# Performance work log

Measured on AMD Instinct MI355X. Metric: run time of the kernel, lower is better.

The kernel has to match this reference:

```python
import jax, jax.numpy as jnp
import numpy as np

DIM = 512
NUM_HEADS = 8


def setup_inputs() -> dict:
    key = jax.random.key(0)
    ks = jax.random.split(key, 10)
    B, N, C = 2, 4096, DIM
    s = 0.02
    return {
        "x": jax.random.normal(ks[0], (B, N, C), dtype=jnp.float32),
        "Wq": jax.random.normal(ks[1], (C, C), dtype=jnp.float32) * s,
        "Wk": jax.random.normal(ks[2], (C, C), dtype=jnp.float32) * s,
        "Wv": jax.random.normal(ks[3], (C, C), dtype=jnp.float32) * s,
        "Wattn": jax.random.normal(ks[4], (C, C), dtype=jnp.float32) * s,
        "Wconv": jax.random.normal(ks[5], (C, C), dtype=jnp.float32) * s,
        "dw_kernel": jax.random.normal(ks[6], (C, 1, 3), dtype=jnp.float32) * s,  # depthwise (O, I/groups, K)
        "dw_bias": jax.random.normal(ks[7], (C,), dtype=jnp.float32) * s,
        "Wcout": jax.random.normal(ks[8], (C, C), dtype=jnp.float32) * s,
        "H": 8,
        "W": 512,
    }


def reference(x, Wq, Wk, Wv, Wattn, Wconv, dw_kernel, dw_bias, Wcout, H, W):
    B, N, C = x.shape
    nh = NUM_HEADS
    hd = C // nh
    scale = hd ** (-0.5)

    # QKV projections (torch Linear: x @ W.T), split heads -> [B, nh, N, hd]
    q = (x @ Wq.T).reshape(B, N, nh, hd).transpose(0, 2, 1, 3)
    k = (x @ Wk.T).reshape(B, N, nh, hd).transpose(0, 2, 1, 3)
    v = (x @ Wv.T).reshape(B, N, nh, hd).transpose(0, 2, 1, 3)

    # Materialized N x N attention (faithful to source)
    scores = jnp.einsum("bhqd,bhkd->bhqk", q, k) * scale
    weights = jax.nn.softmax(scores, axis=-1)
    attn = jnp.einsum("bhqk,bhkd->bhqd", weights, v)
    attn = attn.transpose(0, 2, 1, 3).reshape(B, N, C)
    attn_out = attn @ Wattn.T

    # Parallel depthwise-conv branch
    ci = (x @ Wconv.T).transpose(0, 2, 1)  # [B, C, N]
    co = jax.lax.conv_general_dilated(
        ci, dw_kernel,
        window_strides=(1,), padding=((1, 1),),
        feature_group_count=C,
        dimension_numbers=("NCH", "OIH", "NCH"),
    ) + dw_bias[None, :, None]
    conv_out = co.transpose(0, 2, 1) @ Wcout.T  # [B, N, C]

    out = attn_out + conv_out
    # NOTE: source shadows arg H with num_heads before the view
    return out.reshape(B, nh, W, C)
```

## Files before the change

### kernel.cpp

```cpp
#include <hip/hip_runtime.h>

typedef __attribute__((ext_vector_type(8))) short bf16x8;
typedef __attribute__((ext_vector_type(4))) float f32x4;

constexpr int kB = 2, kN = 4096, kC = 512, kNH = 8, kHD = 64;
constexpr int kBN = kB * kN;
constexpr int kWElems = 262144;
constexpr int kWAll = 6 * kWElems;
constexpr int kWExtra = 3584;
constexpr float kQScale = 0.1803368801f;

__device__ __forceinline__ short f2bf(float f) {
  union { float f; unsigned u; } v; v.f = f;
  unsigned r = v.u + 0x7fffu + ((v.u >> 16) & 1u);
  return (short)(r >> 16);
}
__device__ __forceinline__ float bf2f(short s) {
  union { unsigned u; float f; } v; v.u = ((unsigned)(unsigned short)s) << 16;
  return v.f;
}
__device__ __forceinline__ float exp2_(float x) {
#if __has_builtin(__builtin_amdgcn_exp2f)
  return __builtin_amdgcn_exp2f(x);
#else
  return exp2f(x);
#endif
}
__device__ __forceinline__ unsigned pk2bf(float a, float b) {
  union { float f; unsigned u; } ua, ub; ua.f = a; ub.f = b;
#if __has_builtin(__builtin_amdgcn_perm)
  return __builtin_amdgcn_perm(ub.u + 0x8000u, ua.u + 0x8000u, 0x07060302u);
#else
  return ((ua.u + 0x8000u) >> 16) | (((ub.u + 0x8000u) >> 16) << 16);
#endif
}

__device__ __forceinline__ bf16x8 ld8(const short* p) { return *(const bf16x8*)p; }
__device__ __forceinline__ bf16x8 ld8(const float* p) {
  float4 a = *(const float4*)p;
  float4 b = *(const float4*)(p + 4);
  bf16x8 r;
  r[0] = f2bf(a.x); r[1] = f2bf(a.y); r[2] = f2bf(a.z); r[3] = f2bf(a.w);
  r[4] = f2bf(b.x); r[5] = f2bf(b.y); r[6] = f2bf(b.z); r[7] = f2bf(b.w);
  return r;
}

__device__ __forceinline__ void gload_lds16(const void* g, void* l) {
  __builtin_amdgcn_global_load_lds(
      (const __attribute__((address_space(1))) void*)g,
      (__attribute__((address_space(3))) void*)l, 16, 0, 0);
}

__global__ void detect_dtype(const unsigned* __restrict__ x, int* __restrict__ flag) {
  const int lane = threadIdx.x & 63;
  unsigned w = x[lane];
  int e = (int)((w >> 7) & 0xffu);
  bool bf = (e >= 100 && e <= 140);
  unsigned long long m = __ballot(bf);
  if (lane == 0) *flag = (__popcll(m) >= 32) ? 1 : 0;
}

constexpr int kW8 = kWAll / 8;
constexpr int kX8 = kBN * kC / 8;
__global__ __launch_bounds__(256) void convert_all(
    const void* Wq, const void* Wk, const void* Wv, const void* Wc,
    const void* Wa, const void* Wco, const void* dwk, const void* dwb,
    const void* x, const int* __restrict__ flag, short* __restrict__ dst,
    short* __restrict__ xb) {
  const int gtid = blockIdx.x * 256 + threadIdx.x;
  const bool bf = (*flag != 0);
  if (gtid < kW8) {
    const int e = gtid * 8;
    const int t = e >> 18, off = e & (kWElems - 1);
    const void* src = (t == 0) ? Wq : (t == 1) ? Wk : (t == 2) ? Wv
                    : (t == 3) ? Wc : (t == 4) ? Wa : Wco;
    bf16x8 v = bf ? ld8((const short*)src + off) : ld8((const float*)src + off);
    *(bf16x8*)(dst + e) = v;
  } else if (gtid < kW8 + kWExtra) {
    const int eoff = gtid - kW8;
    if (eoff < 1536) {
      dst[kWAll + eoff] = bf ? ((const short*)dwk)[eoff]
                             : f2bf(((const float*)dwk)[eoff]);
    } else if (eoff < 2048) {
      const int i = eoff - 1536;
      dst[kWAll + 1536 + i] = bf ? ((const short*)dwb)[i]
                                 : f2bf(((const float*)dwb)[i]);
    } else {
      const int t2 = eoff - 2048;
      const int tap = t2 >> 9, c = t2 & 511;
      dst[kWAll + 2048 + t2] = bf ? ((const short*)dwk)[c * 3 + tap]
                                  : f2bf(((const float*)dwk)[c * 3 + tap]);
    }
  } else if (gtid < kW8 + kWExtra + kX8) {
    const int e = (gtid - kW8 - kWExtra) * 8;
    bf16x8 v = bf ? ld8((const short*)x + e) : ld8((const float*)x + e);
    *(bf16x8*)(xb + e) = v;
  }
}

__global__ __launch_bounds__(256, 3) void proj_gemm(
    const short* __restrict__ xb, const short* __restrict__ wb,
    short* __restrict__ q, short* __restrict__ k, short* __restrict__ vT,
    short* __restrict__ ci) {
  __shared__ __align__(16) short Sh[16384];
  short* As = Sh;
  short* Bs = Sh + 8192;
  const int t = threadIdx.x;
  const int wave = t >> 6, lane = t & 63;
  const int row = lane & 15, quad = lane >> 4;
  const int swz = (blockIdx.x & 7) * 128 + (blockIdx.x >> 3);
  const int bn = swz & 15;
  const int bm = swz >> 4;
  const int m0 = bm * 128, n0 = bn * 128;
  const int wm = wave & 1, wn = wave >> 1;
  const int lrow = lane >> 3, lch = lane & 7;

  f32x4 acc[4][4];
#pragma unroll
  for (int mi = 0; mi < 4; ++mi)
#pragma unroll
    for (int ni = 0; ni < 4; ++ni)
#pragma unroll
      for (int r = 0; r < 4; ++r) acc[mi][ni][r] = 0.0f;

  for (int k0 = 0; k0 < kC; k0 += 64) {
#pragma unroll
    for (int p = 0; p < 4; ++p) {
      const int m = wave * 32 + p * 8 + lrow;
      const int kch = lch ^ (m & 7);
      gload_lds16(xb + (size_t)(m0 + m) * kC + k0 + kch * 8,
                  &As[(wave * 32 + p * 8) * 64]);
      gload_lds16(wb + (size_t)(n0 + m) * kC + k0 + kch * 8,
                  &Bs[(wave * 32 + p * 8) * 64]);
    }
    __syncthreads();

#pragma unroll
    for (int kk2 = 0; kk2 < 2; ++kk2) {
      bf16x8 af[4], bfr[4];
#pragma unroll
      for (int mi = 0; mi < 4; ++mi) {
        const int m = wm * 64 + mi * 16 + row;
        const int ch = (kk2 * 4 + quad) ^ (m & 7);
        af[mi] = *(const bf16x8*)(&As[m * 64 + ch * 8]);
      }
#pragma unroll
      for (int ni = 0; ni < 4; ++ni) {
        const int n = wn * 64 + ni * 16 + row;
        const int ch = (kk2 * 4 + quad) ^ (n & 7);
        bfr[ni] = *(const bf16x8*)(&Bs[n * 64 + ch * 8]);
      }
#pragma unroll
      for (int mi = 0; mi < 4; ++mi)
#pragma unroll
        for (int ni = 0; ni < 4; ++ni)
          acc[mi][ni] = __builtin_amdgcn_mfma_f32_16x16x32_bf16(
              af[mi], bfr[ni], acc[mi][ni], 0, 0, 0);
    }
    __syncthreads();
  }

  const int mat = n0 >> 9;
  const float scale = (mat == 0) ? kQScale : 1.0f;
  if (mat != 2) {
#pragma unroll
    for (int mi = 0; mi < 4; ++mi)
#pragma unroll
      for (int ni = 0; ni < 4; ++ni)
#pragma unroll
        for (int r = 0; r < 4; ++r) {
          const int m = wm * 64 + mi * 16 + quad * 4 + r;
          const int n = wn * 64 + ni * 16 + row;
          Sh[m * 128 + (((n >> 3) ^ (m & 15)) * 8) + (n & 7)] =
              f2bf(acc[mi][ni][r] * scale);
        }
  } else {
#pragma unroll
    for (int mi = 0; mi < 4; ++mi)
#pragma unroll
      for (int ni = 0; ni < 4; ++ni)
#pragma unroll
        for (int r = 0; r < 4; ++r) {
          const int m = wm * 64 + mi * 16 + quad * 4 + r;
          const int n = wn * 64 + ni * 16 + row;
          Sh[n * 128 + (((m >> 3) ^ (n & 15)) * 8) + (m & 7)] =
              f2bf(acc[mi][ni][r]);
        }
  }
  __syncthreads();
  const int b_ = m0 >> 12;
  const int rsub = lane >> 4, chk = lane & 15;
#pragma unroll
  for (int i = 0; i < 8; ++i) {
    const int rr = i * 16 + wave * 4 + rsub;
    bf16x8 v = *(const bf16x8*)(&Sh[rr * 128 + ((chk ^ (rr & 15)) * 8)]);
    if (mat == 2) {
      const int cg = (n0 + rr) & 511;
      const int h = cg >> 6, d = cg & 63;
      const int nb = (m0 & (kN - 1)) + chk * 8;
      *(bf16x8*)(vT + ((size_t)((b_ * kNH + h) * kHD + d)) * kN + nb) = v;
    } else {
      const int n_ = (m0 & (kN - 1)) + rr;
      const int cg = (n0 + chk * 8) & 511;
      if (mat == 3) {
        *(bf16x8*)(ci + ((size_t)(b_ * kN + n_)) * kC + cg) = v;
      } else {
        const int h = cg >> 6, d = cg & 63;
        short* dst = (mat == 0) ? q : k;
        *(bf16x8*)(dst + ((size_t)((b_ * kNH + h) * kN + n_)) * kHD + d) = v;
      }
    }
  }
}

__global__ __launch_bounds__(256) void dwconv(
    const short* __restrict__ ci, const short* __restrict__ wb,
    short* __restrict__ cb) {
  const int e0 = (blockIdx.x * 256 + threadIdx.x) * 8;
  const int c0 = e0 & (kC - 1);
  const int bn = e0 >> 9;
  const int n_ = bn & (kN - 1);
  bf16x8 xc = ld8(ci + e0);
  bf16x8 xm, xp;
  if (n_ > 0) xm = ld8(ci + e0 - kC);
  else
#pragma unroll
    for (int i = 0; i < 8; ++i) xm[i] = 0;
  if (n_ < kN - 1) xp = ld8(ci + e0 + kC);
  else
#pragma unroll
    for (int i = 0; i < 8; ++i) xp[i] = 0;
  bf16x8 w0 = ld8(wb + kWAll + 2048 + c0);
  bf16x8 w1 = ld8(wb + kWAll + 2048 + 512 + c0);
  bf16x8 w2 = ld8(wb + kWAll + 2048 + 1024 + c0);
  bf16x8 bi = ld8(wb + kWAll + 1536 + c0);
  bf16x8 o;
#pragma unroll
  for (int i = 0; i < 8; ++i) {
    float a = bf2f(bi[i]) + bf2f(xm[i]) * bf2f(w0[i]) +
              bf2f(xc[i]) * bf2f(w1[i]) + bf2f(xp[i]) * bf2f(w2[i]);
    o[i] = f2bf(a);
  }
  *(bf16x8*)(cb + e0) = o;
}

__global__ __launch_bounds__(512, 2) void attn_flash(
    const short* __restrict__ q, const short* __restrict__ k,
    const short* __restrict__ vT, short* __restrict__ attn) {
  __shared__ __align__(16) short SMEM[69632];
  short* Kb = SMEM;
  short* Vb = SMEM + 32768;
  const int t = threadIdx.x;
  const int wave = t >> 6;
  const int lane = t & 63;
  const int row = lane & 15;
  const int quad = lane >> 4;
  const int qg = wave & 3;
  const int ks = wave >> 2;

  const int slot = blockIdx.x & 7;
  const int inner = blockIdx.x >> 3;
  const int bh = slot * 2 + (inner & 1);
  const int q0 = (inner >> 1) * 256 + qg * 64;

  const short* qbase = q + (size_t)(bh * kN + q0) * kHD;
  const short* kbase = k + (size_t)bh * kN * kHD;
  const short* vbase = vT + (size_t)bh * kHD * kN;

  bf16x8 qb[4][2];
#pragma unroll
  for (int g = 0; g < 4; ++g) {
    qb[g][0] = *(const bf16x8*)(qbase + (g * 16 + row) * kHD + quad * 8);
    qb[g][1] = *(const bf16x8*)(qbase + (g * 16 + row) * kHD + 32 + quad * 8);
  }

  const f32x4 z4 = {0.0f, 0.0f, 0.0f, 0.0f};

  f32x4 o[4][4];
#pragma unroll
  for (int g = 0; g < 4; ++g)
#pragma unroll
    for (int j = 0; j < 4; ++j)
#pragma unroll
      for (int r = 0; r < 4; ++r) o[g][j][r] = 0.0f;
  float l_[4] = {0.0f, 0.0f, 0.0f, 0.0f};

  const int ksrow = lane >> 3;
  const int kschunk = (lane & 7) ^ ksrow;
  auto stage_k = [&](int buf, int ktbase) {
#pragma unroll
    for (int tl = 0; tl < 2; ++tl)
#pragma unroll
      for (int s2 = 0; s2 < 2; ++s2)
        gload_lds16(
            kbase + (size_t)(s2 * 2048 + (ktbase + tl) * 64 + wave * 8 + ksrow) * 64 +
                kschunk * 8,
            &Kb[((buf * 2 + tl) * 2 + s2) * 4096 + wave * 512]);
  };

  const int sv = t >> 8;
  const int ii = t & 255;
  const int i0 = ii, i1 = ii + 256;
  const int sr0 = i0 >> 3, sc0 = i0 & 7;
  const int sr1 = i1 >> 3, sc1 = i1 & 7;
  const int vb0 = (sc0 >> 2) * 32 + (sc0 & 1) * 16 + (sc0 & 2) * 2;
  const int vb1 = (sc1 >> 2) * 32 + (sc1 & 1) * 16 + (sc1 & 2) * 2;

  auto stage_v = [&](int buf, int tl, bf16x8 v0, bf16x8 v1) {
    short* base = &Vb[((buf * 2 + tl) * 2 + sv) * 4608];
    *(short4*)(&base[sr0 * 72 + vb0]) = make_short4(v0[0], v0[1], v0[2], v0[3]);
    *(short4*)(&base[sr0 * 72 + vb0 + 8]) = make_short4(v0[4], v0[5], v0[6], v0[7]);
    *(short4*)(&base[sr1 * 72 + vb1]) = make_short4(v1[0], v1[1], v1[2], v1[3]);
    *(short4*)(&base[sr1 * 72 + vb1 + 8]) = make_short4(v1[4], v1[5], v1[6], v1[7]);
  };

  const int c0s = ((quad) ^ (row & 7)) * 8;
  const int c1s = ((quad + 4) ^ (row & 7)) * 8;

  auto tile_step = [&](const short* kt_base, const short* vt_base) {
    f32x4 s[4][4];
    __builtin_amdgcn_s_setprio(1);
#pragma unroll
    for (int jk = 0; jk < 4; ++jk) {
      const short* kr = kt_base + (jk * 16 + row) * 64;
      bf16x8 a0 = *(const bf16x8*)(kr + c0s);
      bf16x8 a1 = *(const bf16x8*)(kr + c1s);
#pragma unroll
      for (int g = 0; g < 4; ++g) {
        s[g][jk] = __builtin_amdgcn_mfma_f32_16x16x32_bf16(a0, qb[g][0], z4, 0, 0, 0);
        s[g][jk] = __builtin_amdgcn_mfma_f32_16x16x32_bf16(a1, qb[g][1], s[g][jk], 0, 0, 0);
      }
    }
    __builtin_amdgcn_s_setprio(0);

    bf16x8 pb[4][2];
#pragma unroll
    for (int g = 0; g < 4; ++g) {
      float tj[4];
#pragma unroll
      for (int jk = 0; jk < 4; ++jk) {
#pragma unroll
        for (int r = 0; r < 4; ++r) s[g][jk][r] = exp2_(s[g][jk][r]);
        tj[jk] = (s[g][jk][0] + s[g][jk][1]) + (s[g][jk][2] + s[g][jk][3]);
      }
      l_[g] += (tj[0] + tj[1]) + (tj[2] + tj[3]);
#pragma unroll
      for (int c = 0; c < 2; ++c) {
        union { unsigned u[4]; bf16x8 v; } pu;
        pu.u[0] = pk2bf(s[g][2 * c][0], s[g][2 * c][1]);
        pu.u[1] = pk2bf(s[g][2 * c][2], s[g][2 * c][3]);
        pu.u[2] = pk2bf(s[g][2 * c + 1][0], s[g][2 * c + 1][1]);
        pu.u[3] = pk2bf(s[g][2 * c + 1][2], s[g][2 * c + 1][3]);
        pb[g][c] = pu.v;
      }
    }

    __builtin_amdgcn_s_setprio(1);
#pragma unroll
    for (int jd = 0; jd < 4; ++jd) {
      const short* vb = vt_base + (jd * 16 + row) * 72 + quad * 8;
#pragma unroll
      for (int c = 0; c < 2; ++c) {
        bf16x8 av = *(const bf16x8*)(vb + c * 32);
#pragma unroll
        for (int g = 0; g < 4; ++g)
          o[g][jd] = __builtin_amdgcn_mfma_f32_16x16x32_bf16(
              av, pb[g][c], o[g][jd], 0, 0, 0);
      }
    }
    __builtin_amdgcn_s_setprio(0);
  };

  {
    stage_k(0, 0);
#pragma unroll
    for (int tl = 0; tl < 2; ++tl) {
      bf16x8 a = *(const bf16x8*)(vbase + (size_t)sr0 * kN + sv * 2048 + tl * 64 + sc0 * 8);
      bf16x8 b = *(const bf16x8*)(vbase + (size_t)sr1 * kN + sv * 2048 + tl * 64 + sc1 * 8);
      stage_v(0, tl, a, b);
    }
  }
  __syncthreads();

  for (int p = 0; p < 16; ++p) {
    const int cur = p & 1;
    const bool more = (p < 15);
    bf16x8 vn00, vn01, vn10, vn11;
    if (more) {
      stage_k(1 - cur, 2 * p + 2);
      const int off = sv * 2048 + (2 * p + 2) * 64;
      vn00 = *(const bf16x8*)(vbase + (size_t)sr0 * kN + off + sc0 * 8);
      vn01 = *(const bf16x8*)(vbase + (size_t)sr1 * kN + off + sc1 * 8);
      vn10 = *(const bf16x8*)(vbase + (size_t)sr0 * kN + off + 64 + sc0 * 8);
      vn11 = *(const bf16x8*)(vbase + (size_t)sr1 * kN + off + 64 + sc1 * 8);
    }

    tile_step(&Kb[((cur * 2 + 0) * 2 + ks) * 4096], &Vb[((cur * 2 + 0) * 2 + ks) * 4608]);

    if (more) {
      stage_v(1 - cur, 0, vn00, vn01);
      stage_v(1 - cur, 1, vn10, vn11);
    }

    tile_step(&Kb[((cur * 2 + 1) * 2 + ks) * 4096], &Vb[((cur * 2 + 1) * 2 + ks) * 4608]);
    __syncthreads();
  }

  float* Of = (float*)SMEM;
  float* Lf = (float*)SMEM + 16384;
  if (ks == 1) {
#pragma unroll
    for (int g = 0; g < 4; ++g) {
#pragma unroll
      for (int jd = 0; jd < 4; ++jd)
#pragma unroll
        for (int r = 0; r < 4; ++r)
          Of[(g * 16 + jd * 4 + r) * 256 + qg * 64 + lane] = o[g][jd][r];
      Lf[g * 256 + qg * 64 + lane] = l_[g];
    }
  }
  __syncthreads();
  if (ks == 0) {
#pragma unroll
    for (int g = 0; g < 4; ++g) {
#pragma unroll
      for (int jd = 0; jd < 4; ++jd)
#pragma unroll
        for (int r = 0; r < 4; ++r)
          o[g][jd][r] += Of[(g * 16 + jd * 4 + r) * 256 + qg * 64 + lane];
      l_[g] += Lf[g * 256 + qg * 64 + lane];
    }
    const int b_ = bh >> 3, h = bh & 7;
#pragma unroll
    for (int g = 0; g < 4; ++g) {
      float lt = l_[g];
      lt += __shfl_xor(lt, 16);
      lt += __shfl_xor(lt, 32);
      const float linv = 1.0f / lt;
      const int n_ = q0 + g * 16 + row;
      short* ob = attn + (size_t)(b_ * kN + n_) * kC + h * kHD + quad * 4;
#pragma unroll
      for (int jd = 0; jd < 4; ++jd) {
        short4 st = make_short4(f2bf(o[g][jd][0] * linv), f2bf(o[g][jd][1] * linv),
                                f2bf(o[g][jd][2] * linv), f2bf(o[g][jd][3] * linv));
        *(short4*)(ob + jd * 16) = st;
      }
    }
  }
}

template <typename TO>
__device__ __forceinline__ void out_body(
    const short* __restrict__ attn, const short* __restrict__ cb,
    const short* __restrict__ wb, TO* __restrict__ out) {
  __shared__ __align__(16) short Sh[16384];
  short* As = Sh;
  short* Bs = Sh + 8192;
  const int t = threadIdx.x;
  const int wave = t >> 6, lane = t & 63;
  const int row = lane & 15, quad = lane >> 4;
  const int swz = (blockIdx.x & 7) * 64 + (blockIdx.x >> 3);
  const int bn = swz & 7;
  const int bm = swz >> 3;
  const int m0 = bm * 128, n0 = bn * 64;
  const int wm = wave & 1, wn = wave >> 1;
  const int lrow = lane >> 3, lch = lane & 7;

  f32x4 acc[4][2];
#pragma unroll
  for (int mi = 0; mi < 4; ++mi)
#pragma unroll
    for (int ni = 0; ni < 2; ++ni)
#pragma unroll
      for (int r = 0; r < 4; ++r) acc[mi][ni][r] = 0.0f;

  const short* Wa = wb + 4 * kWElems;
  const short* Wo = wb + 5 * kWElems;

  for (int k0 = 0; k0 < 1024; k0 += 64) {
    const short* Asrc = (k0 < 512) ? attn : cb;
    const short* Bsrc = (k0 < 512) ? Wa : Wo;
    const int ka = k0 & 511;
#pragma unroll
    for (int p = 0; p < 4; ++p) {
      const int m = wave * 32 + p * 8 + lrow;
      const int kch = lch ^ (m & 7);
      gload_lds16(Asrc + (size_t)(m0 + m) * kC + ka + kch * 8,
                  &As[(wave * 32 + p * 8) * 64]);
    }
#pragma unroll
    for (int p = 0; p < 2; ++p) {
      const int n = wave * 16 + p * 8 + lrow;
      const int kch = lch ^ (n & 7);
      gload_lds16(Bsrc + (size_t)(n0 + n) * kC + ka + kch * 8,
                  &Bs[(wave * 16 + p * 8) * 64]);
    }
    __syncthreads();

#pragma unroll
    for (int kk2 = 0; kk2 < 2; ++kk2) {
      bf16x8 af[4], bfr[2];
#pragma unroll
      for (int mi = 0; mi < 4; ++mi) {
        const int m = wm * 64 + mi * 16 + row;
        const int ch = (kk2 * 4 + quad) ^ (m & 7);
        af[mi] = *(const bf16x8*)(&As[m * 64 + ch * 8]);
      }
#pragma unroll
      for (int ni = 0; ni < 2; ++ni) {
        const int n = wn * 32 + ni * 16 + row;
        const int ch = (kk2 * 4 + quad) ^ (n & 7);
        bfr[ni] = *(const bf16x8*)(&Bs[n * 64 + ch * 8]);
      }
#pragma unroll
      for (int mi = 0; mi < 4; ++mi)
#pragma unroll
        for (int ni = 0; ni < 2; ++ni)
          acc[mi][ni] = __builtin_amdgcn_mfma_f32_16x16x32_bf16(
              af[mi], bfr[ni], acc[mi][ni], 0, 0, 0);
    }
    __syncthreads();
  }

  if constexpr (sizeof(TO) == 4) {
    float* Shf = (float*)Sh;
#pragma unroll
    for (int mi = 0; mi < 4; ++mi)
#pragma unroll
      for (int ni = 0; ni < 2; ++ni)
#pragma unroll
        for (int r = 0; r < 4; ++r) {
          const int m = wm * 64 + mi * 16 + quad * 4 + r;
          const int n = wn * 32 + ni * 16 + row;
          Shf[m * 64 + (((n >> 2) ^ (m & 15)) * 4) + (n & 3)] = acc[mi][ni][r];
        }
    __syncthreads();
    const int rsub = lane >> 4, chk = lane & 15;
#pragma unroll
    for (int i = 0; i < 8; ++i) {
      const int rr = i * 16 + wave * 4 + rsub;
      float4 v = *(const float4*)(&Shf[rr * 64 + ((chk ^ (rr & 15)) * 4)]);
      *(float4*)((float*)out + (size_t)(m0 + rr) * kC + n0 + chk * 4) = v;
    }
  } else {
#pragma unroll
    for (int mi = 0; mi < 4; ++mi)
#pragma unroll
      for (int ni = 0; ni < 2; ++ni)
#pragma unroll
        for (int r = 0; r < 4; ++r) {
          const int m = wm * 64 + mi * 16 + quad * 4 + r;
          const int n = wn * 32 + ni * 16 + row;
          Sh[m * 64 + (((n >> 3) ^ (m & 7)) * 8) + (n & 7)] =
              f2bf(acc[mi][ni][r]);
        }
    __syncthreads();
    const int rsub = lane >> 3, chk = lane & 7;
#pragma unroll
    for (int i = 0; i < 4; ++i) {
      const int rr = i * 32 + wave * 8 + rsub;
      bf16x8 v = *(const bf16x8*)(&Sh[rr * 64 + ((chk ^ (rr & 7)) * 8)]);
      *(bf16x8*)((short*)out + (size_t)(m0 + rr) * kC + n0 + chk * 8) = v;
    }
  }
}

__global__ __launch_bounds__(256, 4) void out_gemm(
    const short* __restrict__ attn, const short* __restrict__ cb,
    const short* __restrict__ wb, const int* __restrict__ flag, void* out) {
  if (*flag)
    out_body<short>(attn, cb, wb, (short*)out);
  else
    out_body<float>(attn, cb, wb, (float*)out);
}

extern "C" void kernel_launch(void* const* d_in, const int* in_sizes, int n_in,
                              void* d_out, int out_size, void* d_ws, size_t ws_size,
                              hipStream_t stream) {
  const void* x   = d_in[0];
  const void* Wq  = d_in[1];
  const void* Wk  = d_in[2];
  const void* Wv  = d_in[3];
  const void* Wa  = d_in[4];
  const void* Wc  = d_in[5];
  const void* dwk = d_in[6];
  const void* dwb = d_in[7];
  const void* Wco = d_in[8];

  short* ws = (short*)d_ws;
  const size_t E = (size_t)kBN * kC;
  int*   flag = (int*)ws;
  short* wb   = ws + 256;
  short* q    = wb + kWAll + kWExtra;
  short* k    = q + E;
  short* vT   = k + E;
  short* ci   = vT + E;
  short* cb   = ci + E;
  short* attn = ci;
  short* xb   = cb;

  detect_dtype<<<1, 64, 0, stream>>>((const unsigned*)x, flag);
  const int cvt_threads = kW8 + kWExtra + kX8;
  convert_all<<<(cvt_threads + 255) / 256, 256, 0, stream>>>(
      Wq, Wk, Wv, Wc, Wa, Wco, dwk, dwb, x, flag, wb, xb);
  proj_gemm<<<1024, 256, 0, stream>>>(xb, wb, q, k, vT, ci);
  dwconv<<<(kBN * kC) / (256 * 8), 256, 0, stream>>>(ci, wb, cb);
  attn_flash<<<256, 512, 0, stream>>>(q, k, vT, attn);
  out_gemm<<<512, 256, 0, stream>>>(attn, cb, wb, flag, d_out);
}
```

Baseline: 215.6 us.

## Double-buffer LDS in projection and output GEMMs; fold dtype detection into convert

Both the projection GEMM and the output GEMM now use two LDS buffers for their A and B tiles. The next k-tile's global-to-LDS loads are issued before the MFMAs run on the current tile, so load latency overlaps with compute, and the wait between load and use per iteration goes away. This doubles LDS use per block, so the launch-bound occupancy hints drop (3→2 and 4→3). Separately, the detect_dtype launch is removed: each convert_all wave classifies the input dtype itself and thread 0 writes the flag, saving one kernel launch.

```diff
diff --git a/kernel.cpp b/kernel.cpp
--- a/kernel.cpp
+++ b/kernel.cpp
@@ -51,13 +51,12 @@
       (__attribute__((address_space(3))) void*)l, 16, 0, 0);
 }
 
-__global__ void detect_dtype(const unsigned* __restrict__ x, int* __restrict__ flag) {
-  const int lane = threadIdx.x & 63;
-  unsigned w = x[lane];
+__device__ __forceinline__ bool classify_bf(const unsigned* xw) {
+  unsigned w = xw[threadIdx.x & 63];
   int e = (int)((w >> 7) & 0xffu);
-  bool bf = (e >= 100 && e <= 140);
-  unsigned long long m = __ballot(bf);
-  if (lane == 0) *flag = (__popcll(m) >= 32) ? 1 : 0;
+  bool isbf = (e >= 100 && e <= 140);
+  unsigned long long m = __ballot(isbf);
+  return __popcll(m) >= 32;
 }
 
 constexpr int kW8 = kWAll / 8;
@@ -65,10 +64,11 @@
 __global__ __launch_bounds__(256) void convert_all(
     const void* Wq, const void* Wk, const void* Wv, const void* Wc,
     const void* Wa, const void* Wco, const void* dwk, const void* dwb,
-    const void* x, const int* __restrict__ flag, short* __restrict__ dst,
+    const void* x, int* __restrict__ flag, short* __restrict__ dst,
     short* __restrict__ xb) {
+  const bool bf = classify_bf((const unsigned*)x);
   const int gtid = blockIdx.x * 256 + threadIdx.x;
-  const bool bf = (*flag != 0);
+  if (gtid == 0) *flag = bf ? 1 : 0;
   if (gtid < kW8) {
     const int e = gtid * 8;
     const int t = e >> 18, off = e & (kWElems - 1);
@@ -98,13 +98,12 @@
   }
 }
 
-__global__ __launch_bounds__(256, 3) void proj_gemm(
+__global__ __launch_bounds__(256, 2) void proj_gemm(
     const short* __restrict__ xb, const short* __restrict__ wb,
     short* __restrict__ q, short* __restrict__ k, short* __restrict__ vT,
     short* __restrict__ ci) {
-  __shared__ __align__(16) short Sh[16384];
-  short* As = Sh;
-  short* Bs = Sh + 8192;
+  __shared__ __align__(16) short As2[2][8192];
+  __shared__ __align__(16) short Bs2[2][8192];
   const int t = threadIdx.x;
   const int wave = t >> 6, lane = t & 63;
   const int row = lane & 15, quad = lane >> 4;
@@ -123,17 +122,24 @@
 #pragma unroll
       for (int r = 0; r < 4; ++r) acc[mi][ni][r] = 0.0f;
 
-  for (int k0 = 0; k0 < kC; k0 += 64) {
+  auto stage = [&](int buf, int k0) {
 #pragma unroll
     for (int p = 0; p < 4; ++p) {
       const int m = wave * 32 + p * 8 + lrow;
       const int kch = lch ^ (m & 7);
       gload_lds16(xb + (size_t)(m0 + m) * kC + k0 + kch * 8,
-                  &As[(wave * 32 + p * 8) * 64]);
+                  &As2[buf][(wave * 32 + p * 8) * 64]);
       gload_lds16(wb + (size_t)(n0 + m) * kC + k0 + kch * 8,
-                  &Bs[(wave * 32 + p * 8) * 64]);
-    }
-    __syncthreads();
+                  &Bs2[buf][(wave * 32 + p * 8) * 64]);
+    }
+  };
+
+  stage(0, 0);
+  __syncthreads();
+
+  for (int step = 0; step < 8; ++step) {
+    const int cur = step & 1;
+    if (step < 7) stage(1 - cur, (step + 1) * 64);
 
 #pragma unroll
     for (int kk2 = 0; kk2 < 2; ++kk2) {
@@ -142,13 +148,13 @@
       for (int mi = 0; mi < 4; ++mi) {
         const int m = wm * 64 + mi * 16 + row;
         const int ch = (kk2 * 4 + quad) ^ (m & 7);
-        af[mi] = *(const bf16x8*)(&As[m * 64 + ch * 8]);
+        af[mi] = *(const bf16x8*)(&As2[cur][m * 64 + ch * 8]);
       }
 #pragma unroll
       for (int ni = 0; ni < 4; ++ni) {
         const int n = wn * 64 + ni * 16 + row;
         const int ch = (kk2 * 4 + quad) ^ (n & 7);
-        bfr[ni] = *(const bf16x8*)(&Bs[n * 64 + ch * 8]);
+        bfr[ni] = *(const bf16x8*)(&Bs2[cur][n * 64 + ch * 8]);
       }
 #pragma unroll
       for (int mi = 0; mi < 4; ++mi)
@@ -160,6 +166,7 @@
     __syncthreads();
   }
 
+  short* Sh = &As2[0][0];
   const int mat = n0 >> 9;
   const float scale = (mat == 0) ? kQScale : 1.0f;
   if (mat != 2) {
@@ -453,9 +460,8 @@
 __device__ __forceinline__ void out_body(
     const short* __restrict__ attn, const short* __restrict__ cb,
     const short* __restrict__ wb, TO* __restrict__ out) {
-  __shared__ __align__(16) short Sh[16384];
-  short* As = Sh;
-  short* Bs = Sh + 8192;
+  __shared__ __align__(16) short As2[2][8192];
+  __shared__ __align__(16) short Bs2[2][4096];
   const int t = threadIdx.x;
   const int wave = t >> 6, lane = t & 63;
   const int row = lane & 15, quad = lane >> 4;
@@ -477,25 +483,32 @@
   const short* Wa = wb + 4 * kWElems;
   const short* Wo = wb + 5 * kWElems;
 
-  for (int k0 = 0; k0 < 1024; k0 += 64) {
-    const short* Asrc = (k0 < 512) ? attn : cb;
-    const short* Bsrc = (k0 < 512) ? Wa : Wo;
-    const int ka = k0 & 511;
+  auto stage = [&](int buf, int kt) {
+    const short* Asrc = (kt < 8) ? attn : cb;
+    const short* Bsrc = (kt < 8) ? Wa : Wo;
+    const int ka = (kt * 64) & 511;
 #pragma unroll
     for (int p = 0; p < 4; ++p) {
       const int m = wave * 32 + p * 8 + lrow;
       const int kch = lch ^ (m & 7);
       gload_lds16(Asrc + (size_t)(m0 + m) * kC + ka + kch * 8,
-                  &As[(wave * 32 + p * 8) * 64]);
+                  &As2[buf][(wave * 32 + p * 8) * 64]);
     }
 #pragma unroll
     for (int p = 0; p < 2; ++p) {
       const int n = wave * 16 + p * 8 + lrow;
       const int kch = lch ^ (n & 7);
       gload_lds16(Bsrc + (size_t)(n0 + n) * kC + ka + kch * 8,
-                  &Bs[(wave * 16 + p * 8) * 64]);
-    }
-    __syncthreads();
+                  &Bs2[buf][(wave * 16 + p * 8) * 64]);
+    }
+  };
+
+  stage(0, 0);
+  __syncthreads();
+
+  for (int kt = 0; kt < 16; ++kt) {
+    const int cur = kt & 1;
+    if (kt < 15) stage(1 - cur, kt + 1);
 
 #pragma unroll
     for (int kk2 = 0; kk2 < 2; ++kk2) {
@@ -504,13 +517,13 @@
       for (int mi = 0; mi < 4; ++mi) {
         const int m = wm * 64 + mi * 16 + row;
         const int ch = (kk2 * 4 + quad) ^ (m & 7);
-        af[mi] = *(const bf16x8*)(&As[m * 64 + ch * 8]);
+        af[mi] = *(const bf16x8*)(&As2[cur][m * 64 + ch * 8]);
       }
 #pragma unroll
       for (int ni = 0; ni < 2; ++ni) {
         const int n = wn * 32 + ni * 16 + row;
         const int ch = (kk2 * 4 + quad) ^ (n & 7);
-        bfr[ni] = *(const bf16x8*)(&Bs[n * 64 + ch * 8]);
+        bfr[ni] = *(const bf16x8*)(&Bs2[cur][n * 64 + ch * 8]);
       }
 #pragma unroll
       for (int mi = 0; mi < 4; ++mi)
@@ -523,7 +536,7 @@
   }
 
   if constexpr (sizeof(TO) == 4) {
-    float* Shf = (float*)Sh;
+    float* Shf = (float*)&As2[0][0];
 #pragma unroll
     for (int mi = 0; mi < 4; ++mi)
 #pragma unroll
@@ -543,6 +556,7 @@
       *(float4*)((float*)out + (size_t)(m0 + rr) * kC + n0 + chk * 4) = v;
     }
   } else {
+    short* Sh = &As2[0][0];
 #pragma unroll
     for (int mi = 0; mi < 4; ++mi)
 #pragma unroll
@@ -565,7 +579,7 @@
   }
 }
 
-__global__ __launch_bounds__(256, 4) void out_gemm(
+__global__ __launch_bounds__(256, 3) void out_gemm(
     const short* __restrict__ attn, const short* __restrict__ cb,
     const short* __restrict__ wb, const int* __restrict__ flag, void* out) {
   if (*flag)
@@ -599,7 +613,6 @@
   short* attn = ci;
   short* xb   = cb;
 
-  detect_dtype<<<1, 64, 0, stream>>>((const unsigned*)x, flag);
   const int cvt_threads = kW8 + kWExtra + kX8;
   convert_all<<<(cvt_threads + 255) / 256, 256, 0, stream>>>(
       Wq, Wk, Wv, Wc, Wa, Wco, dwk, dwb, x, flag, wb, xb);
```

New measurement: 221.3 us (median of 2 runs). 2.6% more time.
